# Kernel optimization log

Measured on AMD Instinct MI355X. Metric: run time of the kernel, lower is better.

The kernel has to match this reference:

```python
import jax, jax.numpy as jnp
import numpy as np

TAU_MIN, TAU_MAX = 0.02, 2.0
LN_EPS = 1e-5


def setup_inputs() -> dict:
    key = jax.random.key(0)
    ks = jax.random.split(key, 7)
    N, H = 16777216, 16
    neigh3 = jax.random.normal(ks[0], (N, 3), dtype=jnp.float32)
    # LayerNorm(3) affine params
    ln_w = jnp.ones((3,), dtype=jnp.float32)
    ln_b = jnp.zeros((3,), dtype=jnp.float32)
    # Linear(3, 16): torch default init U(-1/sqrt(3), 1/sqrt(3))
    lim1 = 1.0 / np.sqrt(3.0)
    w1 = jax.random.uniform(ks[1], (H, 3), minval=-lim1, maxval=lim1, dtype=jnp.float32)
    b1 = jax.random.uniform(ks[2], (H,), minval=-lim1, maxval=lim1, dtype=jnp.float32)
    # Linear(16, 3)
    lim2 = 1.0 / np.sqrt(float(H))
    w2 = jax.random.uniform(ks[3], (3, H), minval=-lim2, maxval=lim2, dtype=jnp.float32)
    b2 = jax.random.uniform(ks[4], (3,), minval=-lim2, maxval=lim2, dtype=jnp.float32)
    log_tau = jnp.log(jnp.asarray(0.2, dtype=jnp.float32))
    return {"neigh3": neigh3, "ln_w": ln_w, "ln_b": ln_b,
            "w1": w1, "b1": b1, "w2": w2, "b2": b2, "log_tau": log_tau}


def _layernorm(x, w, b):
    mu = jnp.mean(x, axis=-1, keepdims=True)
    var = jnp.mean(jnp.square(x - mu), axis=-1, keepdims=True)
    return (x - mu) * jax.lax.rsqrt(var + LN_EPS) * w + b


def reference(neigh3, ln_w, ln_b, w1, b1, w2, b2, log_tau):
    tau = jnp.clip(jnp.exp(log_tau), TAU_MIN, TAU_MAX)
    # soft-min via -tau * logsumexp(-x/tau) over last dim (size 3)
    best_vals = -tau * jax.nn.logsumexp(-neigh3 / tau, axis=-1)   # [N]
    feats = -jnp.abs(neigh3 - best_vals[..., None])               # [N,3]
    h = _layernorm(feats, ln_w, ln_b)                             # [N,3]
    h = jax.nn.relu(jnp.einsum('nc,hc->nh', h, w1) + b1)          # [N,16]
    logits = jnp.einsum('nh,ch->nc', h, w2) + b2                  # [N,3]
    weights = jax.nn.softmax(logits, axis=-1)
    return jnp.sum(neigh3 * weights, axis=-1)                     # [N]
```

## Files before the change

### kernel.cpp

```cpp
#include <hip/hip_runtime.h>
#include <hip/hip_fp16.h>
#include <math.h>

typedef float vf4 __attribute__((ext_vector_type(4)));
typedef unsigned int u32;

#define LN_EPS 1e-5f
#define NBINS  1024
#define NLUT   (NBINS + 2)


__global__ void nn2_lut_setup(const float* __restrict__ lnw, const float* __restrict__ lnb,
                              const float* __restrict__ w1,  const float* __restrict__ b1,
                              const float* __restrict__ w2,  const float* __restrict__ b2,
                              u32* __restrict__ ws)
{
    int i = blockIdx.x * blockDim.x + threadIdx.x;
    if (i >= NLUT) return;
    int node = i & (NBINS - 1);
    float v  = (float)node * (4.0f / NBINS) - 1.0f;
    float dd = (v <= 1.0f) ? v : (2.0f - v);
    float Pm = 1.0f - fabsf(dd);
    float P  = (v <= 1.0f) ? Pm : -Pm;
    float Q  = dd;
    float n = rsqrtf(P * P + Q * Q);
    float p = 1.7320508075688772f * P * n;
    float q = 1.7320508075688772f * Q * n;
    const float is2 = 0.7071067811865476f;
    const float is6 = 0.4082482904638631f;
    float t0 =  p * is2 + q * is6;
    float t1 = -p * is2 + q * is6;
    float t2 = -2.0f * q * is6;
    float h0 = t0 * lnw[0] + lnb[0];
    float h1 = t1 * lnw[1] + lnb[1];
    float h2 = t2 * lnw[2] + lnb[2];
    float l0 = b2[0], l1 = b2[1], l2 = b2[2];
    for (int j = 0; j < 16; ++j) {
        float a = fmaf(w1[3*j], h0, fmaf(w1[3*j+1], h1, fmaf(w1[3*j+2], h2, b1[j])));
        a = fmaxf(a, 0.0f);
        l0 = fmaf(w2[j],    a, l0);
        l1 = fmaf(w2[16+j], a, l1);
        l2 = fmaf(w2[32+j], a, l2);
    }
    float m  = fmaxf(l0, fmaxf(l1, l2));
    float e0 = expf(l0 - m), e1 = expf(l1 - m), e2 = expf(l2 - m);
    float r  = 1.0f / (e0 + e1 + e2);
    float W0 = e0 * r, W1 = e1 * r;
    u32 pk = ((u32)__half_as_ushort(__float2half_rn(W1)) << 16)
           |  (u32)__half_as_ushort(__float2half_rn(W0));
    ws[i] = pk;
}

__device__ __forceinline__ float row_out(float x0, float x1, float x2,
                                         const u32* lut)
{
    float P   = (x1 - x0) * 1.7320508075688772f;
    float Q   = fmaf(2.0f, x2, -(x0 + x1));
    float den = fabsf(P) + fabsf(Q) + 1e-20f;
    float dd  = Q * __builtin_amdgcn_rcpf(den);
    float v   = (P >= 0.0f) ? dd : (2.0f - dd);
    float u   = fmaf(v, 256.0f, 256.0f);
    int   iu  = (int)u;
    iu = iu < 0 ? 0 : (iu > NBINS ? NBINS : iu);
    float f   = u - (float)iu;
    u32 n0 = lut[iu];
    u32 n1 = lut[iu + 1];
    float a0 = __half2float(__ushort_as_half((unsigned short)(n0 & 0xffffu)));
    float a1 = __half2float(__ushort_as_half((unsigned short)(n0 >> 16)));
    float b0 = __half2float(__ushort_as_half((unsigned short)(n1 & 0xffffu)));
    float b1 = __half2float(__ushort_as_half((unsigned short)(n1 >> 16)));
    float w0 = fmaf(f, b0 - a0, a0);
    float w1 = fmaf(f, b1 - a1, a1);
    return fmaf(w0, x0 - x2, fmaf(w1, x1 - x2, x2));
}

__global__ __launch_bounds__(256) void nn2_lut_main(
    const float* __restrict__ x, const u32* __restrict__ ws,
    float* __restrict__ out, long long nrows, long long T, long long stride)
{
    __shared__ u32 lut[NLUT];
    int tid = threadIdx.x;
    for (int k = tid; k < NLUT; k += 256) lut[k] = ws[k];
    __syncthreads();

    const vf4* x4  = reinterpret_cast<const vf4*>(x);
    vf4*       out4 = reinterpret_cast<vf4*>(out);

    long long grp = (long long)blockIdx.x * 256 + tid;
    if (grp >= T) return;

    vf4 va, vb, vc;
    bool full = (grp * 4 + 4 <= nrows);
    if (full) { va = x4[grp*3]; vb = x4[grp*3 + 1]; vc = x4[grp*3 + 2]; }

    while (true) {
        long long nxt = grp + stride;
        bool nhas = (nxt < T);
        bool nfull = false;
        vf4 na, nb, nc;
        if (nhas) {
            nfull = (nxt * 4 + 4 <= nrows);
            if (nfull) { na = x4[nxt*3]; nb = x4[nxt*3 + 1]; nc = x4[nxt*3 + 2]; }
        }

        if (full) {
            vf4 o;
            o.x = row_out(va.x, va.y, va.z, lut);
            o.y = row_out(va.w, vb.x, vb.y, lut);
            o.z = row_out(vb.z, vb.w, vc.x, lut);
            o.w = row_out(vc.y, vc.z, vc.w, lut);
            __builtin_nontemporal_store(o, &out4[grp]);
        } else {
            for (long long r = grp * 4; r < nrows; ++r)
                out[r] = row_out(x[r*3], x[r*3 + 1], x[r*3 + 2], lut);
        }

        if (!nhas) break;
        grp = nxt; full = nfull; va = na; vb = nb; vc = nc;
    }
}

__global__ __launch_bounds__(256) void nn2_fallback(
    const float* __restrict__ x,
    const float* __restrict__ lnw_g, const float* __restrict__ lnb_g,
    const float* __restrict__ w1_g,  const float* __restrict__ b1_g,
    const float* __restrict__ w2_g,  const float* __restrict__ b2_g,
    float* __restrict__ out, int nrows)
{
    int g = blockIdx.x * blockDim.x + threadIdx.x;
    long long base = (long long)g * 4;
    if (base >= nrows) return;
    const float lw0 = lnw_g[0], lw1 = lnw_g[1], lw2 = lnw_g[2];
    const float lb0 = lnb_g[0], lb1 = lnb_g[1], lb2 = lnb_g[2];
    float X[4][3];
    if (base + 4 <= nrows) {
        const float4* x4 = reinterpret_cast<const float4*>(x) + (long long)g * 3;
        float4 va = x4[0], vb = x4[1], vc = x4[2];
        X[0][0]=va.x; X[0][1]=va.y; X[0][2]=va.z;
        X[1][0]=va.w; X[1][1]=vb.x; X[1][2]=vb.y;
        X[2][0]=vb.z; X[2][1]=vb.w; X[2][2]=vc.x;
        X[3][0]=vc.y; X[3][1]=vc.z; X[3][2]=vc.w;
    } else {
        for (int r = 0; r < 4; ++r) {
            long long rr = (base + r < nrows) ? base + r : (long long)nrows - 1;
            X[r][0]=x[rr*3]; X[r][1]=x[rr*3+1]; X[r][2]=x[rr*3+2];
        }
    }
    float H[4][3];
#pragma unroll
    for (int r = 0; r < 4; ++r) {
        float x0=X[r][0], x1=X[r][1], x2=X[r][2];
        float mu=(x0+x1+x2)*(1.0f/3.0f);
        float d0=mu-x0, d1=mu-x1, d2=mu-x2;
        float rs=__builtin_amdgcn_rsqf(fmaf(fmaf(d0,d0,fmaf(d1,d1,d2*d2)),1.0f/3.0f,LN_EPS));
        H[r][0]=fmaf(d0*rs,lw0,lb0); H[r][1]=fmaf(d1*rs,lw1,lb1); H[r][2]=fmaf(d2*rs,lw2,lb2);
    }
    float L[4][3];
    { const float b20=b2_g[0],b21=b2_g[1],b22=b2_g[2];
#pragma unroll
      for (int r=0;r<4;++r){L[r][0]=b20;L[r][1]=b21;L[r][2]=b22;} }
#pragma unroll
    for (int j = 0; j < 16; ++j) {
        const float a0=w1_g[3*j],a1=w1_g[3*j+1],a2=w1_g[3*j+2],bj=b1_g[j];
        const float u0=w2_g[j],u1=w2_g[16+j],u2=w2_g[32+j];
#pragma unroll
        for (int r=0;r<4;++r){
            float hj=fmaf(H[r][2],a2,fmaf(H[r][1],a1,fmaf(H[r][0],a0,bj)));
            hj=fmaxf(hj,0.0f);
            L[r][0]=fmaf(hj,u0,L[r][0]); L[r][1]=fmaf(hj,u1,L[r][1]); L[r][2]=fmaf(hj,u2,L[r][2]);
        }
    }
    float O[4];
#pragma unroll
    for (int r=0;r<4;++r){
        float l0=L[r][0],l1=L[r][1],l2=L[r][2];
        float lm=fmaxf(l0,fmaxf(l1,l2));
        float s0=__expf(l0-lm),s1=__expf(l1-lm),s2=__expf(l2-lm);
        float rc=__builtin_amdgcn_rcpf(s0+s1+s2);
        O[r]=fmaf(X[r][0],s0,fmaf(X[r][1],s1,X[r][2]*s2))*rc;
    }
    if (base + 4 <= nrows) {
        float4 o; o.x=O[0];o.y=O[1];o.z=O[2];o.w=O[3];
        reinterpret_cast<float4*>(out)[g] = o;
    } else {
        for (int r = 0; r < 4 && base + r < nrows; ++r) out[base + r] = O[r];
    }
}

extern "C" void kernel_launch(void* const* d_in, const int* in_sizes, int n_in,
                              void* d_out, int out_size, void* d_ws, size_t ws_size,
                              hipStream_t stream) {
    const float* x    = (const float*)d_in[0];
    const float* lnw  = (const float*)d_in[1];
    const float* lnb  = (const float*)d_in[2];
    const float* w1   = (const float*)d_in[3];
    const float* b1   = (const float*)d_in[4];
    const float* w2   = (const float*)d_in[5];
    const float* b2   = (const float*)d_in[6];
    float* out = (float*)d_out;
    long long nrows = out_size;

    if (ws_size >= (size_t)NLUT * sizeof(u32)) {
        u32* ws = (u32*)d_ws;
        nn2_lut_setup<<<(NLUT + 255) / 256, 256, 0, stream>>>(lnw, lnb, w1, b1, w2, b2, ws);
        long long T = (nrows + 3) / 4;
        long long need = (T + 255) / 256;
        int grid = (need < 2048) ? (int)need : 2048;
        long long stride = (long long)grid * 256;
        nn2_lut_main<<<grid, 256, 0, stream>>>(x, ws, out, nrows, T, stride);
    } else {
        long long ngroups = (nrows + 3) / 4;
        int grid = (int)((ngroups + 255) / 256);
        nn2_fallback<<<grid, 256, 0, stream>>>(x, lnw, lnb, w1, b1, w2, b2, out, (int)nrows);
    }
}
```

Baseline: 50.06 us.

## Fuse LUT construction into main kernel and stage loads through LDS

Drops the separate LUT setup kernel: every block now builds the 1026-entry softmax-weight LUT in shared memory while its first tile's loads are in flight. Input reads switch from per-thread strided vf4 loads to fully coalesced tile loads, which are staged through LDS and then redistributed so each thread gets its 12 floats, with register double-buffering of the next tile. This removes one launch and the dependency between the two kernels. In exchange, each block repeats the small MLP evaluation, and each tile adds two barriers plus an LDS round trip.

```diff
diff --git a/kernel.cpp b/kernel.cpp
--- a/kernel.cpp
+++ b/kernel.cpp
@@ -10,14 +10,11 @@
 #define NLUT   (NBINS + 2)
 
 
-__global__ void nn2_lut_setup(const float* __restrict__ lnw, const float* __restrict__ lnb,
-                              const float* __restrict__ w1,  const float* __restrict__ b1,
-                              const float* __restrict__ w2,  const float* __restrict__ b2,
-                              u32* __restrict__ ws)
+__device__ __forceinline__ u32 lut_entry(int node,
+    const float* __restrict__ lnw, const float* __restrict__ lnb,
+    const float* __restrict__ w1,  const float* __restrict__ b1,
+    const float* __restrict__ w2,  const float* __restrict__ b2)
 {
-    int i = blockIdx.x * blockDim.x + threadIdx.x;
-    if (i >= NLUT) return;
-    int node = i & (NBINS - 1);
     float v  = (float)node * (4.0f / NBINS) - 1.0f;
     float dd = (v <= 1.0f) ? v : (2.0f - v);
     float Pm = 1.0f - fabsf(dd);
@@ -46,9 +43,8 @@
     float e0 = expf(l0 - m), e1 = expf(l1 - m), e2 = expf(l2 - m);
     float r  = 1.0f / (e0 + e1 + e2);
     float W0 = e0 * r, W1 = e1 * r;
-    u32 pk = ((u32)__half_as_ushort(__float2half_rn(W1)) << 16)
-           |  (u32)__half_as_ushort(__float2half_rn(W0));
-    ws[i] = pk;
+    return ((u32)__half_as_ushort(__float2half_rn(W1)) << 16)
+         |  (u32)__half_as_ushort(__float2half_rn(W0));
 }
 
 __device__ __forceinline__ float row_out(float x0, float x1, float x2,
@@ -74,143 +70,94 @@
     return fmaf(w0, x0 - x2, fmaf(w1, x1 - x2, x2));
 }
 
-__global__ __launch_bounds__(256) void nn2_lut_main(
-    const float* __restrict__ x, const u32* __restrict__ ws,
-    float* __restrict__ out, long long nrows, long long T, long long stride)
+__global__ __launch_bounds__(256) void nn2_fused(
+    const float* __restrict__ x,
+    const float* __restrict__ lnw, const float* __restrict__ lnb,
+    const float* __restrict__ w1,  const float* __restrict__ b1,
+    const float* __restrict__ w2,  const float* __restrict__ b2,
+    float* __restrict__ out, long long nrows, long long ntiles)
 {
     __shared__ u32 lut[NLUT];
-    int tid = threadIdx.x;
-    for (int k = tid; k < NLUT; k += 256) lut[k] = ws[k];
-    __syncthreads();
+    __shared__ vf4 stage[768];
+    const int tid = threadIdx.x;
 
-    const vf4* x4  = reinterpret_cast<const vf4*>(x);
+    const vf4* x4   = reinterpret_cast<const vf4*>(x);
     vf4*       out4 = reinterpret_cast<vf4*>(out);
 
-    long long grp = (long long)blockIdx.x * 256 + tid;
-    if (grp >= T) return;
+    long long tile = blockIdx.x;
+    vf4 r0, r1, r2;
+    bool pfull = false;
+    if (tile < ntiles) {
+        long long gb = tile * 256;
+        pfull = ((gb + 256) * 4 <= nrows);
+        if (pfull) {
+            long long fb = gb * 3;
+            r0 = x4[fb + tid];
+            r1 = x4[fb + tid + 256];
+            r2 = x4[fb + tid + 512];
+        }
+    }
 
-    vf4 va, vb, vc;
-    bool full = (grp * 4 + 4 <= nrows);
-    if (full) { va = x4[grp*3]; vb = x4[grp*3 + 1]; vc = x4[grp*3 + 2]; }
+    for (int i = tid; i < NLUT; i += 256)
+        lut[i] = lut_entry(i & (NBINS - 1), lnw, lnb, w1, b1, w2, b2);
 
-    while (true) {
-        long long nxt = grp + stride;
-        bool nhas = (nxt < T);
-        bool nfull = false;
-        vf4 na, nb, nc;
-        if (nhas) {
-            nfull = (nxt * 4 + 4 <= nrows);
-            if (nfull) { na = x4[nxt*3]; nb = x4[nxt*3 + 1]; nc = x4[nxt*3 + 2]; }
+    for (; tile < ntiles; tile += gridDim.x) {
+        long long gb = tile * 256;
+        bool full = pfull;
+        __syncthreads();
+        if (full) {
+            stage[tid]       = r0;
+            stage[tid + 256] = r1;
+            stage[tid + 512] = r2;
         }
-
+        long long ntile = tile + gridDim.x;
+        pfull = false;
+        if (ntile < ntiles) {
+            long long ngb = ntile * 256;
+            pfull = ((ngb + 256) * 4 <= nrows);
+            if (pfull) {
+                long long fb = ngb * 3;
+                r0 = x4[fb + tid];
+                r1 = x4[fb + tid + 256];
+                r2 = x4[fb + tid + 512];
+            }
+        }
+        __syncthreads();
         if (full) {
+            const vf4* my = &stage[3 * tid];
+            vf4 va = my[0], vb = my[1], vc = my[2];
             vf4 o;
             o.x = row_out(va.x, va.y, va.z, lut);
             o.y = row_out(va.w, vb.x, vb.y, lut);
             o.z = row_out(vb.z, vb.w, vc.x, lut);
             o.w = row_out(vc.y, vc.z, vc.w, lut);
-            __builtin_nontemporal_store(o, &out4[grp]);
+            __builtin_nontemporal_store(o, &out4[gb + tid]);
         } else {
-            for (long long r = grp * 4; r < nrows; ++r)
+            long long grp = gb + tid;
+            long long rbeg = grp * 4;
+            for (long long r = rbeg; r < nrows && r < rbeg + 4; ++r)
                 out[r] = row_out(x[r*3], x[r*3 + 1], x[r*3 + 2], lut);
         }
-
-        if (!nhas) break;
-        grp = nxt; full = nfull; va = na; vb = nb; vc = nc;
-    }
-}
-
-__global__ __launch_bounds__(256) void nn2_fallback(
-    const float* __restrict__ x,
-    const float* __restrict__ lnw_g, const float* __restrict__ lnb_g,
-    const float* __restrict__ w1_g,  const float* __restrict__ b1_g,
-    const float* __restrict__ w2_g,  const float* __restrict__ b2_g,
-    float* __restrict__ out, int nrows)
-{
-    int g = blockIdx.x * blockDim.x + threadIdx.x;
-    long long base = (long long)g * 4;
-    if (base >= nrows) return;
-    const float lw0 = lnw_g[0], lw1 = lnw_g[1], lw2 = lnw_g[2];
-    const float lb0 = lnb_g[0], lb1 = lnb_g[1], lb2 = lnb_g[2];
-    float X[4][3];
-    if (base + 4 <= nrows) {
-        const float4* x4 = reinterpret_cast<const float4*>(x) + (long long)g * 3;
-        float4 va = x4[0], vb = x4[1], vc = x4[2];
-        X[0][0]=va.x; X[0][1]=va.y; X[0][2]=va.z;
-        X[1][0]=va.w; X[1][1]=vb.x; X[1][2]=vb.y;
-        X[2][0]=vb.z; X[2][1]=vb.w; X[2][2]=vc.x;
-        X[3][0]=vc.y; X[3][1]=vc.z; X[3][2]=vc.w;
-    } else {
-        for (int r = 0; r < 4; ++r) {
-            long long rr = (base + r < nrows) ? base + r : (long long)nrows - 1;
-            X[r][0]=x[rr*3]; X[r][1]=x[rr*3+1]; X[r][2]=x[rr*3+2];
-        }
-    }
-    float H[4][3];
-#pragma unroll
-    for (int r = 0; r < 4; ++r) {
-        float x0=X[r][0], x1=X[r][1], x2=X[r][2];
-        float mu=(x0+x1+x2)*(1.0f/3.0f);
-        float d0=mu-x0, d1=mu-x1, d2=mu-x2;
-        float rs=__builtin_amdgcn_rsqf(fmaf(fmaf(d0,d0,fmaf(d1,d1,d2*d2)),1.0f/3.0f,LN_EPS));
-        H[r][0]=fmaf(d0*rs,lw0,lb0); H[r][1]=fmaf(d1*rs,lw1,lb1); H[r][2]=fmaf(d2*rs,lw2,lb2);
-    }
-    float L[4][3];
-    { const float b20=b2_g[0],b21=b2_g[1],b22=b2_g[2];
-#pragma unroll
-      for (int r=0;r<4;++r){L[r][0]=b20;L[r][1]=b21;L[r][2]=b22;} }
-#pragma unroll
-    for (int j = 0; j < 16; ++j) {
-        const float a0=w1_g[3*j],a1=w1_g[3*j+1],a2=w1_g[3*j+2],bj=b1_g[j];
-        const float u0=w2_g[j],u1=w2_g[16+j],u2=w2_g[32+j];
-#pragma unroll
-        for (int r=0;r<4;++r){
-            float hj=fmaf(H[r][2],a2,fmaf(H[r][1],a1,fmaf(H[r][0],a0,bj)));
-            hj=fmaxf(hj,0.0f);
-            L[r][0]=fmaf(hj,u0,L[r][0]); L[r][1]=fmaf(hj,u1,L[r][1]); L[r][2]=fmaf(hj,u2,L[r][2]);
-        }
-    }
-    float O[4];
-#pragma unroll
-    for (int r=0;r<4;++r){
-        float l0=L[r][0],l1=L[r][1],l2=L[r][2];
-        float lm=fmaxf(l0,fmaxf(l1,l2));
-        float s0=__expf(l0-lm),s1=__expf(l1-lm),s2=__expf(l2-lm);
-        float rc=__builtin_amdgcn_rcpf(s0+s1+s2);
-        O[r]=fmaf(X[r][0],s0,fmaf(X[r][1],s1,X[r][2]*s2))*rc;
-    }
-    if (base + 4 <= nrows) {
-        float4 o; o.x=O[0];o.y=O[1];o.z=O[2];o.w=O[3];
-        reinterpret_cast<float4*>(out)[g] = o;
-    } else {
-        for (int r = 0; r < 4 && base + r < nrows; ++r) out[base + r] = O[r];
     }
 }
 
 extern "C" void kernel_launch(void* const* d_in, const int* in_sizes, int n_in,
                               void* d_out, int out_size, void* d_ws, size_t ws_size,
                               hipStream_t stream) {
-    const float* x    = (const float*)d_in[0];
-    const float* lnw  = (const float*)d_in[1];
-    const float* lnb  = (const float*)d_in[2];
-    const float* w1   = (const float*)d_in[3];
-    const float* b1   = (const float*)d_in[4];
-    const float* w2   = (const float*)d_in[5];
-    const float* b2   = (const float*)d_in[6];
+    const float* x   = (const float*)d_in[0];
+    const float* lnw = (const float*)d_in[1];
+    const float* lnb = (const float*)d_in[2];
+    const float* w1  = (const float*)d_in[3];
+    const float* b1  = (const float*)d_in[4];
+    const float* w2  = (const float*)d_in[5];
+    const float* b2  = (const float*)d_in[6];
     float* out = (float*)d_out;
     long long nrows = out_size;
 
-    if (ws_size >= (size_t)NLUT * sizeof(u32)) {
-        u32* ws = (u32*)d_ws;
-        nn2_lut_setup<<<(NLUT + 255) / 256, 256, 0, stream>>>(lnw, lnb, w1, b1, w2, b2, ws);
-        long long T = (nrows + 3) / 4;
-        long long need = (T + 255) / 256;
-        int grid = (need < 2048) ? (int)need : 2048;
-        long long stride = (long long)grid * 256;
-        nn2_lut_main<<<grid, 256, 0, stream>>>(x, ws, out, nrows, T, stride);
-    } else {
-        long long ngroups = (nrows + 3) / 4;
-        int grid = (int)((ngroups + 255) / 256);
-        nn2_fallback<<<grid, 256, 0, stream>>>(x, lnw, lnb, w1, b1, w2, b2, out, (int)nrows);
-    }
+    long long T      = (nrows + 3) / 4;
+    long long ntiles = (T + 255) / 256;
+    int grid = (ntiles < 2048) ? (int)ntiles : 2048;
+
+    nn2_fused<<<grid, 256, 0, stream>>>(x, lnw, lnb, w1, b1, w2, b2,
+                                        out, nrows, ntiles);
 }
```

After: 47.77 us. 1.05x faster.
